# Optimization experiments

Measured on AMD Instinct MI355X. Metric: run time of the kernel, lower is better.

## Reference

```python
import jax, jax.numpy as jnp
import numpy as np

DIM = 1024
HDS = 16
HEAD_DIM = DIM // HDS
ISC = True


def setup_inputs() -> dict:
    key = jax.random.key(0)
    k = jax.random.split(key, 5)
    x = jax.random.normal(k[0], (4, 2048, DIM), dtype=jnp.float32)
    # Linear(dim, 3*dim): weight [3*dim, dim] (torch layout), bias [3*dim]
    scale = 1.0 / np.sqrt(DIM)
    w_qkv = jax.random.uniform(k[1], (3 * DIM, DIM), jnp.float32, -scale, scale)
    b_qkv = jax.random.uniform(k[2], (3 * DIM,), jnp.float32, -scale, scale)
    w_out = jax.random.uniform(k[3], (DIM, DIM), jnp.float32, -scale, scale)
    b_out = jax.random.uniform(k[4], (DIM,), jnp.float32, -scale, scale)
    return {"x": x, "w_qkv": w_qkv, "b_qkv": b_qkv, "w_out": w_out, "b_out": b_out}


def reference(x, w_qkv, b_qkv, w_out, b_out):
    b, s, dim = x.shape
    # QKV projection: x @ w_qkv.T + b_qkv -> split into q, k, v
    qkv = jnp.einsum('bsd,ed->bse', x, w_qkv) + b_qkv
    q, k, v = jnp.split(qkv, 3, axis=-1)
    # [b, s, dim] -> [b, h, s, hd]
    def to_heads(t):
        return t.reshape(b, s, HDS, HEAD_DIM).transpose(0, 2, 1, 3)
    q, k, v = to_heads(q), to_heads(k), to_heads(v)
    att = jnp.einsum('bhqd,bhkd->bhqk', q, k) * (HEAD_DIM ** -0.5)
    if ISC:
        mask = jnp.triu(jnp.ones((s, s), dtype=bool), k=1)  # True above diagonal
        att = jnp.where(mask[None, None], -jnp.inf, att)
    att = jax.nn.softmax(att, axis=-1)
    # dropout is identity in eval mode
    out = jnp.einsum('bhqk,bhkd->bhqd', att, v)
    out = out.transpose(0, 2, 1, 3).reshape(b, s, dim)
    out = jnp.einsum('bsd,ed->bse', out, w_out) + b_out
    return out
```

## Files before the change

kernel.cpp:

```cpp
#include <hip/hip_runtime.h>
#include <stdint.h>

typedef __bf16 bf16x8 __attribute__((ext_vector_type(8)));
typedef short s16x8 __attribute__((ext_vector_type(8)));
typedef short s16x4 __attribute__((ext_vector_type(4)));
typedef float f32x4 __attribute__((ext_vector_type(4)));
typedef unsigned short u16;

#define K_DIM 1024

static __device__ __forceinline__ u16 f2bf(float f) {
    uint32_t x = __float_as_uint(f);
    x += 0x7fffu + ((x >> 16) & 1u);
    return (u16)(x >> 16);
}

static __device__ __forceinline__ f32x4 mfma16(s16x8 a, s16x8 b, f32x4 c) {
    return __builtin_amdgcn_mfma_f32_16x16x32_bf16(
        __builtin_bit_cast(bf16x8, a), __builtin_bit_cast(bf16x8, b), c, 0, 0, 0);
}

static __device__ __forceinline__ void gload16(const u16* g, u16* l) {
    __builtin_amdgcn_global_load_lds(
        (const __attribute__((address_space(1))) void*)g,
        (__attribute__((address_space(3))) void*)l,
        16, 0, 0);
}

static __device__ __forceinline__ uint32_t cvt_pk_bf16(float lo, float hi) {
    uint32_t r;
    asm("v_cvt_pk_bf16_f32 %0, %1, %2" : "=v"(r) : "v"(lo), "v"(hi));
    return r;
}

static __device__ __forceinline__ float fexp2(float x) {
#if __has_builtin(__builtin_amdgcn_exp2f)
    return __builtin_amdgcn_exp2f(x);
#else
    return __expf(x * 0.69314718056f);
#endif
}

__global__ void cvt_all(const float* __restrict__ x, const float* __restrict__ wq,
                        const float* __restrict__ wo,
                        u16* __restrict__ xb, u16* __restrict__ wqb,
                        u16* __restrict__ wob) {
    const int stride = gridDim.x * blockDim.x;
    const int tid = blockIdx.x * blockDim.x + threadIdx.x;
    for (int i = tid; i < 2097152; i += stride) {
        float4 f = ((const float4*)x)[i];
        ushort4 o;
        o.x = f2bf(f.x); o.y = f2bf(f.y); o.z = f2bf(f.z); o.w = f2bf(f.w);
        ((ushort4*)xb)[i] = o;
    }
    for (int i = tid; i < 786432; i += stride) {
        float4 f = ((const float4*)wq)[i];
        ushort4 o;
        o.x = f2bf(f.x); o.y = f2bf(f.y); o.z = f2bf(f.z); o.w = f2bf(f.w);
        ((ushort4*)wqb)[i] = o;
    }
    for (int i = tid; i < 262144; i += stride) {
        float4 f = ((const float4*)wo)[i];
        ushort4 o;
        o.x = f2bf(f.x); o.y = f2bf(f.y); o.z = f2bf(f.z); o.w = f2bf(f.w);
        ((ushort4*)wob)[i] = o;
    }
}

__global__ __launch_bounds__(256) void gemm_qkv(
    const u16* __restrict__ A, const u16* __restrict__ B,
    const float* __restrict__ bias,
    u16* __restrict__ qo, u16* __restrict__ ko, u16* __restrict__ vto)
{
    __shared__ u16 smem[32768];
    u16* ct = smem;
    const int tid = threadIdx.x;
    const int w = tid >> 6, l = tid & 63;
    const int lr = l & 15, lc = l >> 4;

    const int f = blockIdx.y * 64 + blockIdx.x;
    const int c = f & 7, j = f >> 3;
    const int m0 = (c * 8 + (j & 7)) * 128;
    const int n0 = (j >> 3) * 128;
    const int wm = (w >> 1) * 64, wn = (w & 1) * 64;

    const int srow = w * 8 + (l >> 3);
    const int scol = ((l & 7) ^ (l >> 3)) * 8;
    const u16* gA = A + (size_t)(m0 + srow) * K_DIM + scol;
    const u16* gB = B + (size_t)(n0 + srow) * K_DIM + scol;

    f32x4 acc[4][4] = {};

    auto stage = [&](int k0, int buf) {
        u16* base = smem + buf * 16384;
        #pragma unroll
        for (int g = 0; g < 4; ++g) {
            gload16(gA + (size_t)g * 32 * K_DIM + k0, base + (g * 32 + w * 8) * 64);
            gload16(gB + (size_t)g * 32 * K_DIM + k0, base + 8192 + (g * 32 + w * 8) * 64);
        }
    };

    stage(0, 0);
    int cur = 0;

    for (int k0 = 0; k0 < K_DIM; k0 += 64) {
        __syncthreads();
        if (k0 + 64 < K_DIM) stage(k0 + 64, cur ^ 1);
        const u16* As = smem + cur * 16384;
        const u16* Bs = As + 8192;
        #pragma unroll
        for (int kk = 0; kk < 2; ++kk) {
            s16x8 a[4], b[4];
            #pragma unroll
            for (int i = 0; i < 4; ++i) {
                const int row = wm + i * 16 + lr;
                a[i] = *(const s16x8*)&As[row * 64 + ((kk * 32 + lc * 8) ^ ((row & 7) * 8))];
            }
            #pragma unroll
            for (int jn = 0; jn < 4; ++jn) {
                const int row = wn + jn * 16 + lr;
                b[jn] = *(const s16x8*)&Bs[row * 64 + ((kk * 32 + lc * 8) ^ ((row & 7) * 8))];
            }
            #pragma unroll
            for (int i = 0; i < 4; ++i)
                #pragma unroll
                for (int jn = 0; jn < 4; ++jn)
                    acc[i][jn] = mfma16(a[i], b[jn], acc[i][jn]);
        }
        cur ^= 1;
    }

    const int sec = n0 >> 10;
    const int bb = m0 >> 11, s0 = m0 & 2047;

    if (sec < 2) {
        #pragma unroll
        for (int jn = 0; jn < 4; ++jn) {
            const int n = n0 + wn + jn * 16 + lr;
            const float bv = bias[n];
            const int h = (n & 1023) >> 6, d = n & 63;
            #pragma unroll
            for (int i = 0; i < 4; ++i) {
                #pragma unroll
                for (int r = 0; r < 4; ++r) {
                    const int m = m0 + wm + i * 16 + lc * 4 + r;
                    const int s = m & 2047;
                    float v = acc[i][jn][r] + bv;
                    if (sec == 0)
                        qo[((size_t)((bb * 16 + h) * 2048 + s)) * 64 + d] = f2bf(v * 0.18033688f);
                    else
                        ko[((size_t)((bb * 16 + h) * 2048 + s)) * 64 + d] = f2bf(v);
                }
            }
        }
    } else {
        __syncthreads();
        #pragma unroll
        for (int jj = 0; jj < 4; ++jj) {
            const int nl = (wn >> 6) * 16 + lr;
            const float bv = bias[n0 + wn + jj * 16 + lr];
            #pragma unroll
            for (int i = 0; i < 4; ++i) {
                const int mloc = wm + i * 16 + lc * 4;
                uint2 pk;
                pk.x = cvt_pk_bf16(acc[i][jj][0] + bv, acc[i][jj][1] + bv);
                pk.y = cvt_pk_bf16(acc[i][jj][2] + bv, acc[i][jj][3] + bv);
                *(s16x4*)&ct[nl * 136 + mloc] = __builtin_bit_cast(s16x4, pk);
            }
            __syncthreads();
            #pragma unroll
            for (int rep = 0; rep < 2; ++rep) {
                const int col = tid >> 3;
                const int seg = (tid & 7) + rep * 8;
                const int nn = n0 + (col >> 4) * 64 + jj * 16 + (col & 15);
                const int h = (nn & 1023) >> 6, d = nn & 63;
                const int mo = seg * 8;
                s16x8 v = *(const s16x8*)&ct[col * 136 + mo];
                *(s16x8*)&vto[((size_t)((bb * 16 + h) * 64 + d)) * 2048 + s0 + mo] = v;
            }
            __syncthreads();
        }
    }
}

__global__ __launch_bounds__(256, 2) void attn_fwd(
    const u16* __restrict__ q, const u16* __restrict__ k,
    const u16* __restrict__ vt, u16* __restrict__ ao)
{
    __shared__ u16 kt[2][8 * 512];
    __shared__ u16 vtl[2][8 * 512];
    __shared__ u16 plds[4 * 32 * 72];
    const int w = threadIdx.x >> 6, l = threadIdx.x & 63;
    const int lr = l & 15, lc = l >> 4;
    const int bh = blockIdx.x;
    const int cp = blockIdx.y;
    const u16* qp = q + (size_t)bh * 2048 * 64;
    const u16* kp = k + (size_t)bh * 2048 * 64;
    const u16* vp = vt + (size_t)bh * 64 * 2048;
    u16* pl = &plds[w * 2304];
    const int bb = bh >> 4, h = bh & 15;

    for (int pass = 0; pass < 2; ++pass) {
        const int C = pass ? (15 - cp) : cp;
        const int q0 = C * 128 + w * 32;
        const int nb = 2 * C + 2;
        const int diag = 2 * C + (w >> 1);

        s16x8 aQ[2][2];
        #pragma unroll
        for (int i = 0; i < 2; ++i)
            #pragma unroll
            for (int kk = 0; kk < 2; ++kk)
                aQ[i][kk] = *(const s16x8*)&qp[(q0 + i * 16 + lr) * 64 + kk * 32 + lc * 8];

        f32x4 O[2][4] = {};
        f32x4 lsv[2] = {};

        auto stage = [&](int t, int buf) {
            const int c0 = t * 64;
            if (w < 2) {
                #pragma unroll
                for (int gi = 0; gi < 4; ++gi) {
                    const int g = w * 4 + gi;
                    const int jx = g >> 1, kk = g & 1;
                    gload16(kp + (c0 + jx * 16 + lr) * 64 + kk * 32 + lc * 8,
                            &kt[buf][g * 512]);
                }
            } else {
                #pragma unroll
                for (int gi = 0; gi < 4; ++gi) {
                    const int g = (w - 2) * 4 + gi;
                    const int jd = g >> 1, kk = g & 1;
                    gload16(vp + (jd * 16 + lr) * 2048 + c0 + kk * 32 + lc * 8,
                            &vtl[buf][g * 512]);
                }
            }
        };

        __syncthreads();
        stage(0, 0);
        int cur = 0;

        for (int t = 0; t < nb; ++t) {
            __syncthreads();
            if (t + 1 < nb) stage(t + 1, cur ^ 1);

            if (t <= diag) {
                const int c0 = t * 64;
                f32x4 s[2][4] = {};
                __builtin_amdgcn_s_setprio(1);
                #pragma unroll
                for (int jx = 0; jx < 4; ++jx) {
                    s16x8 k0 = *(const s16x8*)&kt[cur][(jx * 2 + 0) * 512 + l * 8];
                    s16x8 k1 = *(const s16x8*)&kt[cur][(jx * 2 + 1) * 512 + l * 8];
                    s[0][jx] = mfma16(k0, aQ[0][0], s[0][jx]);
                    s[0][jx] = mfma16(k1, aQ[0][1], s[0][jx]);
                    s[1][jx] = mfma16(k0, aQ[1][0], s[1][jx]);
                    s[1][jx] = mfma16(k1, aQ[1][1], s[1][jx]);
                }
                __builtin_amdgcn_s_setprio(0);
                if (t == diag) {
                    #pragma unroll
                    for (int i = 0; i < 2; ++i) {
                        const int qrow = q0 + i * 16 + lr;
                        #pragma unroll
                        for (int jx = 0; jx < 4; ++jx) {
                            const int kvb = c0 + jx * 16 + lc * 4;
                            #pragma unroll
                            for (int r = 0; r < 4; ++r)
                                if (kvb + r > qrow) s[i][jx][r] = -1e30f;
                        }
                    }
                }
                #pragma unroll
                for (int i = 0; i < 2; ++i) {
                    #pragma unroll
                    for (int jx = 0; jx < 4; ++jx)
                        #pragma unroll
                        for (int r = 0; r < 4; ++r)
                            s[i][jx][r] = fexp2(s[i][jx][r]);
                    lsv[i] += (s[i][0] + s[i][1]) + (s[i][2] + s[i][3]);
                    #pragma unroll
                    for (int jx = 0; jx < 4; ++jx) {
                        uint2 pk;
                        pk.x = cvt_pk_bf16(s[i][jx][0], s[i][jx][1]);
                        pk.y = cvt_pk_bf16(s[i][jx][2], s[i][jx][3]);
                        *(s16x4*)&pl[(i * 16 + lr) * 72 + jx * 16 + lc * 4] =
                            __builtin_bit_cast(s16x4, pk);
                    }
                }
                s16x8 aP[2][2];
                #pragma unroll
                for (int i = 0; i < 2; ++i)
                    #pragma unroll
                    for (int kk = 0; kk < 2; ++kk)
                        aP[i][kk] = *(const s16x8*)&pl[(i * 16 + lr) * 72 + kk * 32 + lc * 8];
                __builtin_amdgcn_s_setprio(1);
                #pragma unroll
                for (int jd = 0; jd < 4; ++jd) {
                    s16x8 v0 = *(const s16x8*)&vtl[cur][(jd * 2 + 0) * 512 + l * 8];
                    s16x8 v1 = *(const s16x8*)&vtl[cur][(jd * 2 + 1) * 512 + l * 8];
                    O[0][jd] = mfma16(aP[0][0], v0, O[0][jd]);
                    O[0][jd] = mfma16(aP[0][1], v1, O[0][jd]);
                    O[1][jd] = mfma16(aP[1][0], v0, O[1][jd]);
                    O[1][jd] = mfma16(aP[1][1], v1, O[1][jd]);
                }
                __builtin_amdgcn_s_setprio(0);
            }
            cur ^= 1;
        }

        float lsr[2];
        #pragma unroll
        for (int i = 0; i < 2; ++i) {
            float t2 = (lsv[i][0] + lsv[i][1]) + (lsv[i][2] + lsv[i][3]);
            t2 += __shfl_xor(t2, 16);
            t2 += __shfl_xor(t2, 32);
            lsr[i] = 1.0f / t2;
        }
        float inv[2][4];
        #pragma unroll
        for (int i = 0; i < 2; ++i)
            #pragma unroll
            for (int r = 0; r < 4; ++r)
                inv[i][r] = __shfl(lsr[i], lc * 4 + r);

        #pragma unroll
        for (int i = 0; i < 2; ++i)
            #pragma unroll
            for (int jd = 0; jd < 4; ++jd)
                #pragma unroll
                for (int r = 0; r < 4; ++r) {
                    const int srow = q0 + i * 16 + lc * 4 + r;
                    ao[((size_t)(bb * 2048 + srow)) * 1024 + h * 64 + jd * 16 + lr] =
                        f2bf(O[i][jd][r] * inv[i][r]);
                }
    }
}

__global__ __launch_bounds__(256) void gemm_out(
    const u16* __restrict__ A, const u16* __restrict__ B,
    const float* __restrict__ bias, float* __restrict__ out)
{
    __shared__ u16 smem[32768];
    const int tid = threadIdx.x;
    const int w = tid >> 6, l = tid & 63;
    const int lr = l & 15, lc = l >> 4;

    const int f = blockIdx.y * 64 + blockIdx.x;
    const int c = f & 7, j = f >> 3;
    const int m0 = (c * 8 + (j & 7)) * 128;
    const int n0 = (j >> 3) * 128;
    const int wm = (w >> 1) * 64, wn = (w & 1) * 64;

    const int srow = w * 8 + (l >> 3);
    const int scol = ((l & 7) ^ (l >> 3)) * 8;
    const u16* gA = A + (size_t)(m0 + srow) * K_DIM + scol;
    const u16* gB = B + (size_t)(n0 + srow) * K_DIM + scol;

    f32x4 acc[4][4] = {};

    auto stage = [&](int k0, int buf) {
        u16* base = smem + buf * 16384;
        #pragma unroll
        for (int g = 0; g < 4; ++g) {
            gload16(gA + (size_t)g * 32 * K_DIM + k0, base + (g * 32 + w * 8) * 64);
            gload16(gB + (size_t)g * 32 * K_DIM + k0, base + 8192 + (g * 32 + w * 8) * 64);
        }
    };

    stage(0, 0);
    int cur = 0;

    for (int k0 = 0; k0 < K_DIM; k0 += 64) {
        __syncthreads();
        if (k0 + 64 < K_DIM) stage(k0 + 64, cur ^ 1);
        const u16* As = smem + cur * 16384;
        const u16* Bs = As + 8192;
        #pragma unroll
        for (int kk = 0; kk < 2; ++kk) {
            s16x8 a[4], b[4];
            #pragma unroll
            for (int i = 0; i < 4; ++i) {
                const int row = wm + i * 16 + lr;
                a[i] = *(const s16x8*)&As[row * 64 + ((kk * 32 + lc * 8) ^ ((row & 7) * 8))];
            }
            #pragma unroll
            for (int jn = 0; jn < 4; ++jn) {
                const int row = wn + jn * 16 + lr;
                b[jn] = *(const s16x8*)&Bs[row * 64 + ((kk * 32 + lc * 8) ^ ((row & 7) * 8))];
            }
            #pragma unroll
            for (int i = 0; i < 4; ++i)
                #pragma unroll
                for (int jn = 0; jn < 4; ++jn)
                    acc[i][jn] = mfma16(a[i], b[jn], acc[i][jn]);
        }
        cur ^= 1;
    }

    #pragma unroll
    for (int jn = 0; jn < 4; ++jn) {
        const int n = n0 + wn + jn * 16 + lr;
        const float bv = bias[n];
        #pragma unroll
        for (int i = 0; i < 4; ++i) {
            #pragma unroll
            for (int r = 0; r < 4; ++r) {
                const int m = m0 + wm + i * 16 + lc * 4 + r;
                out[(size_t)m * 1024 + n] = acc[i][jn][r] + bv;
            }
        }
    }
}

extern "C" void kernel_launch(void* const* d_in, const int* in_sizes, int n_in,
                              void* d_out, int out_size, void* d_ws, size_t ws_size,
                              hipStream_t stream) {
    const float* x     = (const float*)d_in[0];
    const float* w_qkv = (const float*)d_in[1];
    const float* b_qkv = (const float*)d_in[2];
    const float* w_out = (const float*)d_in[3];
    const float* b_out = (const float*)d_in[4];
    float* out = (float*)d_out;

    char* ws = (char*)d_ws;
    u16* xb   = (u16*)(ws);
    u16* wqb  = (u16*)(ws + 16777216);
    u16* wob  = (u16*)(ws + 23068672);
    u16* qws  = (u16*)(ws + 25165824);
    u16* kws  = (u16*)(ws + 41943040);
    u16* vtws = (u16*)(ws + 58720256);
    u16* attn = (u16*)(ws + 75497472);

    cvt_all<<<dim3(2048), 256, 0, stream>>>(x, w_qkv, w_out, xb, wqb, wob);

    gemm_qkv<<<dim3(64, 24), 256, 0, stream>>>(xb, wqb, b_qkv, qws, kws, vtws);
    attn_fwd<<<dim3(64, 8), 256, 0, stream>>>(qws, kws, vtws, attn);
    gemm_out<<<dim3(64, 8), 256, 0, stream>>>(attn, wob, b_out, out);
}
```

Measured before the change: 132.7 us.

## Switch attention to 32x32x16 MFMA and keep P in registers via permlane swap

The attention kernel moves from 16x16x32 to 32x32x16 bf16 MFMA tiles, and the K/V staging layouts are rearranged to match. The probability tile is no longer written to and read back from LDS. Instead it is repacked in registers with v_permlane32_swap so the S accumulator layout can feed straight in as the A operand of the PV MFMA. This removes the per-tile LDS round trip and its shared memory, at the cost of new lane-layout assumptions and larger accumulator register use.

```diff
diff --git a/kernel.cpp b/kernel.cpp
--- a/kernel.cpp
+++ b/kernel.cpp
@@ -5,6 +5,7 @@
 typedef short s16x8 __attribute__((ext_vector_type(8)));
 typedef short s16x4 __attribute__((ext_vector_type(4)));
 typedef float f32x4 __attribute__((ext_vector_type(4)));
+typedef float f32x16 __attribute__((ext_vector_type(16)));
 typedef unsigned short u16;
 
 #define K_DIM 1024
@@ -17,6 +18,11 @@
 
 static __device__ __forceinline__ f32x4 mfma16(s16x8 a, s16x8 b, f32x4 c) {
     return __builtin_amdgcn_mfma_f32_16x16x32_bf16(
+        __builtin_bit_cast(bf16x8, a), __builtin_bit_cast(bf16x8, b), c, 0, 0, 0);
+}
+
+static __device__ __forceinline__ f32x16 mfma32(s16x8 a, s16x8 b, f32x16 c) {
+    return __builtin_amdgcn_mfma_f32_32x32x16_bf16(
         __builtin_bit_cast(bf16x8, a), __builtin_bit_cast(bf16x8, b), c, 0, 0, 0);
 }
 
@@ -31,6 +37,10 @@
     uint32_t r;
     asm("v_cvt_pk_bf16_f32 %0, %1, %2" : "=v"(r) : "v"(lo), "v"(hi));
     return r;
+}
+
+static __device__ __forceinline__ void pswap(uint32_t& a, uint32_t& b) {
+    asm volatile("v_permlane32_swap_b32 %0, %1" : "+v"(a), "+v"(b));
 }
 
 static __device__ __forceinline__ float fexp2(float x) {
@@ -189,16 +199,14 @@
 {
     __shared__ u16 kt[2][8 * 512];
     __shared__ u16 vtl[2][8 * 512];
-    __shared__ u16 plds[4 * 32 * 72];
     const int w = threadIdx.x >> 6, l = threadIdx.x & 63;
-    const int lr = l & 15, lc = l >> 4;
+    const int l31 = l & 31, hl = l >> 5;
     const int bh = blockIdx.x;
     const int cp = blockIdx.y;
     const u16* qp = q + (size_t)bh * 2048 * 64;
     const u16* kp = k + (size_t)bh * 2048 * 64;
     const u16* vp = vt + (size_t)bh * 64 * 2048;
-    u16* pl = &plds[w * 2304];
-    const int bb = bh >> 4, h = bh & 15;
+    const int bb = bh >> 4, hd = bh & 15;
 
     for (int pass = 0; pass < 2; ++pass) {
         const int C = pass ? (15 - cp) : cp;
@@ -206,15 +214,13 @@
         const int nb = 2 * C + 2;
         const int diag = 2 * C + (w >> 1);
 
-        s16x8 aQ[2][2];
-        #pragma unroll
-        for (int i = 0; i < 2; ++i)
-            #pragma unroll
-            for (int kk = 0; kk < 2; ++kk)
-                aQ[i][kk] = *(const s16x8*)&qp[(q0 + i * 16 + lr) * 64 + kk * 32 + lc * 8];
-
-        f32x4 O[2][4] = {};
-        f32x4 lsv[2] = {};
+        s16x8 aQ[4];
+        #pragma unroll
+        for (int kk = 0; kk < 4; ++kk)
+            aQ[kk] = *(const s16x8*)&qp[(q0 + l31) * 64 + kk * 16 + hl * 8];
+
+        f32x16 O[2] = {};
+        f32x16 ls16 = {};
 
         auto stage = [&](int t, int buf) {
             const int c0 = t * 64;
@@ -222,16 +228,16 @@
                 #pragma unroll
                 for (int gi = 0; gi < 4; ++gi) {
                     const int g = w * 4 + gi;
-                    const int jx = g >> 1, kk = g & 1;
-                    gload16(kp + (c0 + jx * 16 + lr) * 64 + kk * 32 + lc * 8,
+                    const int jx = g >> 2, kk = g & 3;
+                    gload16(kp + (c0 + jx * 32 + l31) * 64 + kk * 16 + hl * 8,
                             &kt[buf][g * 512]);
                 }
             } else {
                 #pragma unroll
                 for (int gi = 0; gi < 4; ++gi) {
                     const int g = (w - 2) * 4 + gi;
-                    const int jd = g >> 1, kk = g & 1;
-                    gload16(vp + (jd * 16 + lr) * 2048 + c0 + kk * 32 + lc * 8,
+                    const int jd = g >> 2, ks = g & 3;
+                    gload16(vp + (jd * 32 + l31) * 2048 + c0 + ks * 16 + hl * 8,
                             &vtl[buf][g * 512]);
                 }
             }
@@ -247,94 +253,77 @@
 
             if (t <= diag) {
                 const int c0 = t * 64;
-                f32x4 s[2][4] = {};
+                f32x16 s[2] = {};
                 __builtin_amdgcn_s_setprio(1);
                 #pragma unroll
-                for (int jx = 0; jx < 4; ++jx) {
-                    s16x8 k0 = *(const s16x8*)&kt[cur][(jx * 2 + 0) * 512 + l * 8];
-                    s16x8 k1 = *(const s16x8*)&kt[cur][(jx * 2 + 1) * 512 + l * 8];
-                    s[0][jx] = mfma16(k0, aQ[0][0], s[0][jx]);
-                    s[0][jx] = mfma16(k1, aQ[0][1], s[0][jx]);
-                    s[1][jx] = mfma16(k0, aQ[1][0], s[1][jx]);
-                    s[1][jx] = mfma16(k1, aQ[1][1], s[1][jx]);
-                }
+                for (int jx = 0; jx < 2; ++jx)
+                    #pragma unroll
+                    for (int kk = 0; kk < 4; ++kk) {
+                        s16x8 kf = *(const s16x8*)&kt[cur][(jx * 4 + kk) * 512 + l * 8];
+                        s[jx] = mfma32(kf, aQ[kk], s[jx]);
+                    }
                 __builtin_amdgcn_s_setprio(0);
                 if (t == diag) {
+                    const int qrow = q0 + l31;
                     #pragma unroll
-                    for (int i = 0; i < 2; ++i) {
-                        const int qrow = q0 + i * 16 + lr;
+                    for (int jx = 0; jx < 2; ++jx)
                         #pragma unroll
-                        for (int jx = 0; jx < 4; ++jx) {
-                            const int kvb = c0 + jx * 16 + lc * 4;
-                            #pragma unroll
-                            for (int r = 0; r < 4; ++r)
-                                if (kvb + r > qrow) s[i][jx][r] = -1e30f;
+                        for (int reg = 0; reg < 16; ++reg) {
+                            const int kv = c0 + jx * 32 + (reg & 3) + 8 * (reg >> 2) + 4 * hl;
+                            if (kv > qrow) s[jx][reg] = -1e30f;
                         }
+                }
+                #pragma unroll
+                for (int jx = 0; jx < 2; ++jx)
+                    #pragma unroll
+                    for (int reg = 0; reg < 16; ++reg)
+                        s[jx][reg] = fexp2(s[jx][reg]);
+                ls16 += s[0] + s[1];
+                s16x8 ap[4];
+                #pragma unroll
+                for (int ks = 0; ks < 4; ++ks) {
+                    const int jxs = ks >> 1, b8 = (ks & 1) * 8;
+                    uint32_t XA = cvt_pk_bf16(s[jxs][b8 + 0], s[jxs][b8 + 1]);
+                    uint32_t XB = cvt_pk_bf16(s[jxs][b8 + 2], s[jxs][b8 + 3]);
+                    uint32_t YA = cvt_pk_bf16(s[jxs][b8 + 4], s[jxs][b8 + 5]);
+                    uint32_t YB = cvt_pk_bf16(s[jxs][b8 + 6], s[jxs][b8 + 7]);
+                    pswap(XA, YA);
+                    pswap(XB, YB);
+                    uint4 wds = make_uint4(XA, XB, YA, YB);
+                    ap[ks] = __builtin_bit_cast(s16x8, wds);
+                }
+                __builtin_amdgcn_s_setprio(1);
+                #pragma unroll
+                for (int jd = 0; jd < 2; ++jd)
+                    #pragma unroll
+                    for (int ks = 0; ks < 4; ++ks) {
+                        s16x8 vf = *(const s16x8*)&vtl[cur][(jd * 4 + ks) * 512 + l * 8];
+                        O[jd] = mfma32(ap[ks], vf, O[jd]);
                     }
-                }
-                #pragma unroll
-                for (int i = 0; i < 2; ++i) {
-                    #pragma unroll
-                    for (int jx = 0; jx < 4; ++jx)
-                        #pragma unroll
-                        for (int r = 0; r < 4; ++r)
-                            s[i][jx][r] = fexp2(s[i][jx][r]);
-                    lsv[i] += (s[i][0] + s[i][1]) + (s[i][2] + s[i][3]);
-                    #pragma unroll
-                    for (int jx = 0; jx < 4; ++jx) {
-                        uint2 pk;
-                        pk.x = cvt_pk_bf16(s[i][jx][0], s[i][jx][1]);
-                        pk.y = cvt_pk_bf16(s[i][jx][2], s[i][jx][3]);
-                        *(s16x4*)&pl[(i * 16 + lr) * 72 + jx * 16 + lc * 4] =
-                            __builtin_bit_cast(s16x4, pk);
-                    }
-                }
-                s16x8 aP[2][2];
-                #pragma unroll
-                for (int i = 0; i < 2; ++i)
-                    #pragma unroll
-                    for (int kk = 0; kk < 2; ++kk)
-                        aP[i][kk] = *(const s16x8*)&pl[(i * 16 + lr) * 72 + kk * 32 + lc * 8];
-                __builtin_amdgcn_s_setprio(1);
-                #pragma unroll
-                for (int jd = 0; jd < 4; ++jd) {
-                    s16x8 v0 = *(const s16x8*)&vtl[cur][(jd * 2 + 0) * 512 + l * 8];
-                    s16x8 v1 = *(const s16x8*)&vtl[cur][(jd * 2 + 1) * 512 + l * 8];
-                    O[0][jd] = mfma16(aP[0][0], v0, O[0][jd]);
-                    O[0][jd] = mfma16(aP[0][1], v1, O[0][jd]);
-                    O[1][jd] = mfma16(aP[1][0], v0, O[1][jd]);
-                    O[1][jd] = mfma16(aP[1][1], v1, O[1][jd]);
-                }
                 __builtin_amdgcn_s_setprio(0);
             }
             cur ^= 1;
         }
 
-        float lsr[2];
-        #pragma unroll
-        for (int i = 0; i < 2; ++i) {
-            float t2 = (lsv[i][0] + lsv[i][1]) + (lsv[i][2] + lsv[i][3]);
-            t2 += __shfl_xor(t2, 16);
-            t2 += __shfl_xor(t2, 32);
-            lsr[i] = 1.0f / t2;
-        }
-        float inv[2][4];
-        #pragma unroll
-        for (int i = 0; i < 2; ++i)
-            #pragma unroll
-            for (int r = 0; r < 4; ++r)
-                inv[i][r] = __shfl(lsr[i], lc * 4 + r);
-
-        #pragma unroll
-        for (int i = 0; i < 2; ++i)
-            #pragma unroll
-            for (int jd = 0; jd < 4; ++jd)
-                #pragma unroll
-                for (int r = 0; r < 4; ++r) {
-                    const int srow = q0 + i * 16 + lc * 4 + r;
-                    ao[((size_t)(bb * 2048 + srow)) * 1024 + h * 64 + jd * 16 + lr] =
-                        f2bf(O[i][jd][r] * inv[i][r]);
-                }
+        float t2 = 0.f;
+        #pragma unroll
+        for (int e = 0; e < 16; ++e) t2 += ls16[e];
+        t2 += __shfl_xor(t2, 32);
+        const float lsr = 1.0f / t2;
+
+        float invr[16];
+        #pragma unroll
+        for (int reg = 0; reg < 16; ++reg)
+            invr[reg] = __shfl(lsr, (reg & 3) + 8 * (reg >> 2) + 4 * hl);
+
+        #pragma unroll
+        for (int jd = 0; jd < 2; ++jd)
+            #pragma unroll
+            for (int reg = 0; reg < 16; ++reg) {
+                const int qr = (reg & 3) + 8 * (reg >> 2) + 4 * hl;
+                ao[((size_t)(bb * 2048 + q0 + qr)) * 1024 + hd * 64 + jd * 32 + l31] =
+                    f2bf(O[jd][reg] * invr[reg]);
+            }
     }
 }
 
```

Result: no change. 133.0 us (+0.2%).
